# Kernel tuning notes

Measured on AMD Instinct MI355X. Metric: run time of the kernel, lower is better.

The kernel has to match this reference:

```python
import jax, jax.numpy as jnp
import numpy as np

H = 8        # attention heads
G = 8        # groupnorm groups
EPS = 1e-5

def mish(x):
    return x * jnp.tanh(jnp.logaddexp(x, 0.0))

def conv1d(x, w, b, pad):
    # x: [B,C,L], w: [O,I,K]
    y = jax.lax.conv_general_dilated(x, w, (1,), [(pad, pad)],
                                     dimension_numbers=('NCH', 'OIH', 'NCH'))
    return y + b[None, :, None]

def gn_per_step(x, gamma, beta):
    # torch code reshapes [B,C,L] -> [(B L), C] and applies GroupNorm(G, C):
    # normalize each (b, l) position over channel groups.
    B, C, L = x.shape
    xg = x.reshape(B, G, C // G, L)
    mean = xg.mean(axis=2, keepdims=True)
    var = xg.var(axis=2, keepdims=True)
    xg = (xg - mean) * jax.lax.rsqrt(var + EPS)
    return xg.reshape(B, C, L) * gamma[None, :, None] + beta[None, :, None]

def layernorm(x, g, b):
    mean = x.mean(axis=-1, keepdims=True)
    var = x.var(axis=-1, keepdims=True)
    return (x - mean) * jax.lax.rsqrt(var + EPS) * g + b


def setup_inputs() -> dict:
    key = jax.random.key(0)
    ks = jax.random.split(key, 16)
    B, Cin, Cout, L, N, CD, TD = 64, 256, 512, 512, 77, 768, 512
    w = lambda k, shape, s=0.02: (jax.random.normal(k, shape, jnp.float32) * s)
    return {
        'x': jax.random.normal(ks[0], (B, Cin, L), jnp.float32),
        't': jax.random.normal(ks[1], (B, TD), jnp.float32),
        'cond': jax.random.normal(ks[2], (B, N, CD), jnp.float32),
        'conv0_w': w(ks[3], (Cout, Cin, 5)), 'conv0_b': jnp.zeros((Cout,), jnp.float32),
        'gn0_g': jnp.ones((Cout,), jnp.float32), 'gn0_b': jnp.zeros((Cout,), jnp.float32),
        'tm_w': w(ks[4], (2 * Cout, TD)), 'tm_b': jnp.zeros((2 * Cout,), jnp.float32),
        'conv1_w': w(ks[5], (Cout, Cout, 5)), 'conv1_b': jnp.zeros((Cout,), jnp.float32),
        'gn1_g': jnp.ones((Cout,), jnp.float32), 'gn1_b': jnp.zeros((Cout,), jnp.float32),
        'res_w': w(ks[6], (Cout, Cin, 1)), 'res_b': jnp.zeros((Cout,), jnp.float32),
        'ln_x_g': jnp.ones((Cout,), jnp.float32), 'ln_x_b': jnp.zeros((Cout,), jnp.float32),
        'ln_c_g': jnp.ones((CD,), jnp.float32), 'ln_c_b': jnp.zeros((CD,), jnp.float32),
        'q_w': w(ks[7], (Cout, Cout)), 'q_b': jnp.zeros((Cout,), jnp.float32),
        'k_w': w(ks[8], (Cout, CD)), 'k_b': jnp.zeros((Cout,), jnp.float32),
        'v_w': w(ks[9], (Cout, CD)), 'v_b': jnp.zeros((Cout,), jnp.float32),
        'cond_indices': jnp.arange(B, dtype=jnp.int64 if jax.config.jax_enable_x64 else jnp.int32),
    }


def _forward(x, t, cond,
             conv0_w, conv0_b, gn0_g, gn0_b, tm_w, tm_b,
             conv1_w, conv1_b, gn1_g, gn1_b, res_w, res_b,
             ln_x_g, ln_x_b, ln_c_g, ln_c_b,
             q_w, q_b, k_w, k_b, v_w, v_b, cond_indices):
    Cout = conv0_w.shape[0]
    # ---- ResidualTemporalBlock (adagn=True) ----
    ss = jnp.einsum('bi,oi->bo', mish(t), tm_w) + tm_b        # [B, 2*Cout]
    scale = ss[:, :Cout, None]                                 # chunk dim=1
    shift = ss[:, Cout:, None]
    h = conv1d(x, conv0_w, conv0_b, pad=2)                     # [B,Cout,L]
    h = gn_per_step(h, gn0_g, gn0_b)
    h = mish(h * (1.0 + scale) + shift)                        # ada_shift_scale + Mish
    h = conv1d(h, conv1_w, conv1_b, pad=2)
    h = mish(gn_per_step(h, gn1_g, gn1_b))
    out = h + conv1d(x, res_w, res_b, pad=0)                   # residual 1x1 conv
    # ---- ResidualCrossAttentionLayer (LinearCrossAttention) ----
    xs = out[cond_indices]                                     # [Bc,Cout,L]
    xi = xs.transpose(0, 2, 1)                                 # [Bc,L,Cout]
    cs = cond[cond_indices]                                    # [Bc,N,CD]
    Bc, T, D = xi.shape
    Nn = cs.shape[1]
    Dh = D // H
    q = jnp.einsum('btl,dl->btd', layernorm(xi, ln_x_g, ln_x_b), q_w) + q_b
    cn = layernorm(cs, ln_c_g, ln_c_b)
    k = jnp.einsum('bnl,dl->bnd', cn, k_w) + k_b
    v = jnp.einsum('bnl,dl->bnd', cn, v_w) + v_b
    q = jax.nn.softmax(q.reshape(Bc, T, H, Dh), axis=-1)       # softmax over head dim
    k = jax.nn.softmax(k.reshape(Bc, Nn, H, Dh), axis=1)       # softmax over tokens
    v = v.reshape(Bc, Nn, H, Dh)
    attn = jnp.einsum('bnhd,bnhl->bhdl', k, v)                 # [Bc,H,Dh,Dh] kernel
    y = jnp.einsum('bthd,bhdl->bthl', q, attn).reshape(Bc, T, D)
    return out.at[cond_indices].add(y.transpose(0, 2, 1))


def reference(x, t, cond,
              conv0_w, conv0_b, gn0_g, gn0_b, tm_w, tm_b,
              conv1_w, conv1_b, gn1_g, gn1_b, res_w, res_b,
              ln_x_g, ln_x_b, ln_c_g, ln_c_b,
              q_w, q_b, k_w, k_b, v_w, v_b, cond_indices):
    return _forward(x, t, cond, conv0_w, conv0_b, gn0_g, gn0_b, tm_w, tm_b,
                    conv1_w, conv1_b, gn1_g, gn1_b, res_w, res_b,
                    ln_x_g, ln_x_b, ln_c_g, ln_c_b,
                    q_w, q_b, k_w, k_b, v_w, v_b, cond_indices)
```

## Files before the change

### kernel.cpp

```cpp
#include <hip/hip_runtime.h>
#include <math.h>

#define EPS 1e-5f

typedef __attribute__((ext_vector_type(8))) short short8;
typedef __attribute__((ext_vector_type(4))) float floatx4;

typedef __attribute__((address_space(1))) const void* gas1_t;
typedef __attribute__((address_space(3))) void* las3_t;

__device__ __forceinline__ void glls16(const void* g, void* l) {
    __builtin_amdgcn_global_load_lds((gas1_t)g, (las3_t)l, 16, 0, 0);
}

__device__ __forceinline__ float mishf(float x) {
    float sp = fmaxf(x, 0.0f) + log1pf(expf(-fabsf(x)));
    return x * tanhf(sp);
}
__device__ __forceinline__ unsigned short f2bf(float f) {
    unsigned int u = __float_as_uint(f);
    unsigned int r = (u + 0x7fffu + ((u >> 16) & 1u)) >> 16;
    return (unsigned short)r;
}
__device__ __forceinline__ float bf2f(unsigned short s) {
    return __uint_as_float(((unsigned int)s) << 16);
}
__device__ __forceinline__ unsigned int pk2(unsigned short a, unsigned short b) {
    return (unsigned int)a | ((unsigned int)b << 16);
}

__global__ __launch_bounds__(256) void setup_k(
        const float* __restrict__ conv0_w, const float* __restrict__ conv1_w,
        const float* __restrict__ res_w, const float* __restrict__ q_w,
        const float* __restrict__ k_w, const float* __restrict__ v_w,
        const float* __restrict__ t,
        unsigned short* __restrict__ wp0, unsigned short* __restrict__ wp1,
        unsigned short* __restrict__ wr, unsigned short* __restrict__ wq,
        unsigned short* __restrict__ wk, unsigned short* __restrict__ wvv,
        float* __restrict__ mt,
        unsigned short* __restrict__ xTp, unsigned short* __restrict__ h0Tp) {
    const int blk = blockIdx.x, tid = threadIdx.x;
    if (blk < 2560) {
        int o = blk * 256 + tid;
        int ci = o & 255, co = (o >> 8) & 511, kk = o >> 17;
        wp0[o] = f2bf(conv0_w[((size_t)co * 256 + ci) * 5 + kk]);
    } else if (blk < 7680) {
        int o = (blk - 2560) * 256 + tid;
        int ci = o & 511, co = (o >> 9) & 511, kk = o >> 18;
        wp1[o] = f2bf(conv1_w[((size_t)co * 512 + ci) * 5 + kk]);
    } else if (blk < 7808) {
        int i = (blk - 7680) * 256 + tid;
        float4 f = *(const float4*)&res_w[(size_t)i * 4];
        *(uint2*)&wr[(size_t)i * 4] =
            make_uint2(pk2(f2bf(f.x), f2bf(f.y)), pk2(f2bf(f.z), f2bf(f.w)));
    } else if (blk < 8064) {
        int i = (blk - 7808) * 256 + tid;
        float4 f = *(const float4*)&q_w[(size_t)i * 4];
        *(uint2*)&wq[(size_t)i * 4] =
            make_uint2(pk2(f2bf(f.x), f2bf(f.y)), pk2(f2bf(f.z), f2bf(f.w)));
    } else if (blk < 8448) {
        int i = (blk - 8064) * 256 + tid;
        float4 f = *(const float4*)&k_w[(size_t)i * 4];
        *(uint2*)&wk[(size_t)i * 4] =
            make_uint2(pk2(f2bf(f.x), f2bf(f.y)), pk2(f2bf(f.z), f2bf(f.w)));
    } else if (blk < 8832) {
        int i = (blk - 8448) * 256 + tid;
        float4 f = *(const float4*)&v_w[(size_t)i * 4];
        *(uint2*)&wvv[(size_t)i * 4] =
            make_uint2(pk2(f2bf(f.x), f2bf(f.y)), pk2(f2bf(f.z), f2bf(f.w)));
    } else if (blk < 8960) {
        int i = (blk - 8832) * 256 + tid;
        mt[i] = mishf(t[i]);
    } else if (blk < 8992) {
        int idx = (blk - 8960) * 256 + tid;
        int u = idx * 8;
        int c = u & 255, r4 = (u >> 8) & 3, b = u >> 10;
        int row = (r4 < 2) ? r4 : (512 + r4);
        *(uint4*)&xTp[((size_t)b * 516 + row) * 256 + c] = make_uint4(0, 0, 0, 0);
    } else {
        int idx = (blk - 8992) * 256 + tid;
        int u = idx * 8;
        int c = u & 511, r4 = (u >> 9) & 3, b = u >> 11;
        int row = (r4 < 2) ? r4 : (512 + r4);
        *(uint4*)&h0Tp[((size_t)b * 516 + row) * 512 + c] = make_uint4(0, 0, 0, 0);
    }
}

__global__ __launch_bounds__(256) void xpose_cvt(const float* __restrict__ x,
        unsigned short* __restrict__ xT) {
    __shared__ float tile[64][68];
    const int tid = threadIdx.x;
    const int l0 = blockIdx.x * 64, c0 = blockIdx.y * 64, b = blockIdx.z;
    for (int idx = tid; idx < 64 * 16; idx += 256) {
        int cr = idx >> 4, lc = (idx & 15) * 4;
        float4 f = *(const float4*)&x[((size_t)b * 256 + c0 + cr) * 512 + l0 + lc];
        tile[cr][lc] = f.x; tile[cr][lc + 1] = f.y;
        tile[cr][lc + 2] = f.z; tile[cr][lc + 3] = f.w;
    }
    __syncthreads();
    for (int idx = tid; idx < 64 * 16; idx += 256) {
        int lr = idx >> 4, cc = (idx & 15) * 4;
        *(uint2*)&xT[((size_t)b * 516 + 2 + l0 + lr) * 256 + c0 + cc] =
            make_uint2(pk2(f2bf(tile[cc][lr]), f2bf(tile[cc + 1][lr])),
                       pk2(f2bf(tile[cc + 2][lr]), f2bf(tile[cc + 3][lr])));
    }
}

template<int KD>
__global__ __launch_bounds__(256) void gemm_nt(const float* __restrict__ A,
        const float* __restrict__ W, const float* __restrict__ bias,
        float* __restrict__ C, int M, int N) {
    constexpr int ST = 20;
    __shared__ __align__(16) float As[64 * ST];
    __shared__ __align__(16) float Ws[64 * ST];
    const int tid = threadIdx.x;
    const int r0 = blockIdx.x * 64, c0 = blockIdx.y * 64;
    const int tx = tid & 15, ty = tid >> 4;
    const int lrow = tid >> 2, lk = (tid & 3) * 4;
    float acc[4][4];
#pragma unroll
    for (int i = 0; i < 4; ++i)
#pragma unroll
        for (int j = 0; j < 4; ++j) acc[i][j] = 0.f;
    for (int k0 = 0; k0 < KD; k0 += 16) {
        __syncthreads();
        *(float4*)&As[lrow * ST + lk] =
            *(const float4*)&A[(size_t)(r0 + lrow) * KD + k0 + lk];
        *(float4*)&Ws[lrow * ST + lk] =
            *(const float4*)&W[(size_t)(c0 + lrow) * KD + k0 + lk];
        __syncthreads();
#pragma unroll
        for (int kk = 0; kk < 16; kk += 4) {
            float4 av[4], wv[4];
#pragma unroll
            for (int i = 0; i < 4; ++i)
                av[i] = *(const float4*)&As[(ty + 16 * i) * ST + kk];
#pragma unroll
            for (int j = 0; j < 4; ++j)
                wv[j] = *(const float4*)&Ws[(tx + 16 * j) * ST + kk];
#pragma unroll
            for (int i = 0; i < 4; ++i)
#pragma unroll
                for (int j = 0; j < 4; ++j) {
                    acc[i][j] = fmaf(av[i].x, wv[j].x, acc[i][j]);
                    acc[i][j] = fmaf(av[i].y, wv[j].y, acc[i][j]);
                    acc[i][j] = fmaf(av[i].z, wv[j].z, acc[i][j]);
                    acc[i][j] = fmaf(av[i].w, wv[j].w, acc[i][j]);
                }
        }
    }
#pragma unroll
    for (int j = 0; j < 4; ++j) {
        int c = c0 + tx + 16 * j;
        float bv = bias[c];
#pragma unroll
        for (int i = 0; i < 4; ++i)
            C[(size_t)(r0 + ty + 16 * i) * N + c] = acc[i][j] + bv;
    }
}

template<int CI, bool FILM, bool OPAD>
__global__ __launch_bounds__(256) void conv5_mfma(
        const unsigned short* __restrict__ xb,
        const unsigned short* __restrict__ wp,
        const float* __restrict__ bias,
        const float* __restrict__ gam, const float* __restrict__ bet,
        const float* __restrict__ ss,
        unsigned short* __restrict__ outT) {
    constexpr int NC = CI / 32;
    __shared__ __align__(16) unsigned short xs[2][260 * 32];
    __shared__ __align__(16) unsigned short wsm[2][5 * 64 * 32];
    __shared__ float sgam[64], sbet[64], sbias[64], sscale[64], sshift[64];

    const int tid = threadIdx.x;
    const int l0 = blockIdx.x * 256;
    const int co0 = blockIdx.y * 64;
    const int b = blockIdx.z;
    const int lane = tid & 63;
    const int wv = tid >> 6;
    const int lq = lane & 15, qd = lane >> 4;
    const int wn = wv * 64;

    if (tid < 64) {
        int co = co0 + tid;
        sbias[tid] = bias[co];
        sgam[tid] = gam[co];
        sbet[tid] = bet[co];
        if (FILM) {
            sscale[tid] = ss[(size_t)b * 1024 + co];
            sshift[tid] = ss[(size_t)b * 1024 + 512 + co];
        }
    }

    const unsigned short* gxb = xb + ((size_t)b * 516 + l0) * CI;
    const unsigned short* gwb = wp + (size_t)co0 * CI;

    const unsigned short* xsp[5];
    const unsigned short* wsp[5];
    unsigned sdo[5];
#pragma unroll
    for (int it = 0; it < 5; ++it) {
        int task = it * 256 + tid;
        {
            int ri = task >> 2, pos = task & 3;
            int seg = pos ^ ((ri >> 1) & 3);
            xsp[it] = gxb + (size_t)ri * CI + seg * 8;
        }
        {
            int kk = task >> 8, r = task & 255;
            int col = r >> 2, pos = r & 3;
            int seg = pos ^ ((col >> 1) & 3);
            wsp[it] = gwb + ((size_t)kk * 512 + col) * CI + seg * 8;
        }
        sdo[it] = (unsigned)(it * 256 + wn) * 8;
    }
    const bool xv4 = tid < 16;

    auto stage = [&](int buf) {
#pragma unroll
        for (int it = 0; it < 5; ++it) {
            if (it < 4 || xv4) glls16(xsp[it], &xs[buf][sdo[it]]);
            xsp[it] += 32;
        }
#pragma unroll
        for (int it = 0; it < 5; ++it) {
            glls16(wsp[it], &wsm[buf][sdo[it]]);
            wsp[it] += 32;
        }
    };

    unsigned bvo[5][4], avo[5][4];
#pragma unroll
    for (int kk = 0; kk < 5; ++kk) {
#pragma unroll
        for (int j = 0; j < 4; ++j) {
            int row = wn + j * 16 + lq + kk;
            int pos = qd ^ ((row >> 1) & 3);
            bvo[kk][j] = (unsigned)(row * 32 + pos * 8) * 2u;
        }
#pragma unroll
        for (int i = 0; i < 4; ++i) {
            int crow = i * 16 + lq;
            int pos = qd ^ ((crow >> 1) & 3);
            avo[kk][i] = (unsigned)(kk * 2048 + crow * 32 + pos * 8) * 2u;
        }
    }

    floatx4 acc[4][4];
#pragma unroll
    for (int i = 0; i < 4; ++i)
#pragma unroll
        for (int j = 0; j < 4; ++j) acc[i][j] = (floatx4){0.f, 0.f, 0.f, 0.f};

    auto compute = [&](int buf) {
        const char* xr = (const char*)xs[buf];
        const char* wr_ = (const char*)wsm[buf];
#pragma unroll
        for (int kk = 0; kk < 5; ++kk) {
            short8 bvf[4];
#pragma unroll
            for (int j = 0; j < 4; ++j)
                bvf[j] = *(const short8*)(xr + bvo[kk][j]);
#pragma unroll
            for (int i = 0; i < 4; ++i) {
                short8 av = *(const short8*)(wr_ + avo[kk][i]);
#pragma unroll
                for (int j = 0; j < 4; ++j)
                    acc[i][j] = __builtin_amdgcn_mfma_f32_16x16x32_bf16(
                        av, bvf[j], acc[i][j], 0, 0, 0);
            }
        }
    };

    stage(0);
    __syncthreads();
#pragma unroll 1
    for (int c = 0; c < NC; c += 2) {
        stage(1);
        compute(0);
        __syncthreads();
        if (c + 2 < NC) stage(0);
        compute(1);
        __syncthreads();
    }

    float m_[4], rs_[4];
#pragma unroll
    for (int j = 0; j < 4; ++j) {
        float s1 = 0.f, s2 = 0.f;
#pragma unroll
        for (int i = 0; i < 4; ++i) {
            float4 bv4 = *(const float4*)&sbias[i * 16 + qd * 4];
            float ba[4] = {bv4.x, bv4.y, bv4.z, bv4.w};
#pragma unroll
            for (int r = 0; r < 4; ++r) {
                float v = acc[i][j][r] + ba[r];
                acc[i][j][r] = v;
                s1 += v; s2 += v * v;
            }
        }
        s1 += __shfl_xor(s1, 16, 64); s2 += __shfl_xor(s2, 16, 64);
        s1 += __shfl_xor(s1, 32, 64); s2 += __shfl_xor(s2, 32, 64);
        float mean = s1 * (1.f / 64.f);
        float var = s2 * (1.f / 64.f) - mean * mean;
        m_[j] = mean; rs_[j] = rsqrtf(var + EPS);
    }
#pragma unroll
    for (int j = 0; j < 4; ++j) {
        int l = l0 + wn + j * 16 + lq;
        size_t rowbase = OPAD ? (((size_t)b * 516 + 2 + l) * 512 + co0)
                              : (((size_t)b * 512 + l) * 512 + co0);
#pragma unroll
        for (int i = 0; i < 4; ++i) {
            float4 g4 = *(const float4*)&sgam[i * 16 + qd * 4];
            float4 b4 = *(const float4*)&sbet[i * 16 + qd * 4];
            float ga[4] = {g4.x, g4.y, g4.z, g4.w};
            float be[4] = {b4.x, b4.y, b4.z, b4.w};
            float sa[4] = {0, 0, 0, 0}, sh[4] = {0, 0, 0, 0};
            if (FILM) {
                float4 s4 = *(const float4*)&sscale[i * 16 + qd * 4];
                float4 h4 = *(const float4*)&sshift[i * 16 + qd * 4];
                sa[0] = s4.x; sa[1] = s4.y; sa[2] = s4.z; sa[3] = s4.w;
                sh[0] = h4.x; sh[1] = h4.y; sh[2] = h4.z; sh[3] = h4.w;
            }
            unsigned short o[4];
#pragma unroll
            for (int r = 0; r < 4; ++r) {
                float v = (acc[i][j][r] - m_[j]) * rs_[j] * ga[r] + be[r];
                if (FILM) v = v * (1.f + sa[r]) + sh[r];
                o[r] = f2bf(mishf(v));
            }
            *(uint2*)&outT[rowbase + i * 16 + qd * 4] =
                make_uint2(pk2(o[0], o[1]), pk2(o[2], o[3]));
        }
    }
}

template<int KD, int EPI, bool PADA>
__global__ __launch_bounds__(256) void gemm1_mfma(
        const unsigned short* __restrict__ A,
        const unsigned short* __restrict__ W,
        const float* __restrict__ bias,
        const unsigned short* __restrict__ addT,
        float* __restrict__ outF,
        unsigned short* __restrict__ outB,
        int Mreal) {
    constexpr int NC = KD / 32;
    __shared__ __align__(16) unsigned short xs[2][256 * 32];
    __shared__ __align__(16) unsigned short wsm[2][64 * 32];
    __shared__ float sbias[64];
    const int tid = threadIdx.x;
    const int m0 = blockIdx.x * 256;
    const int n0 = blockIdx.y * 64;
    const int lane = tid & 63;
    const int wv = tid >> 6;
    const int lq = lane & 15, qd = lane >> 4;
    const int wn = wv * 64;
    if (tid < 64) sbias[tid] = bias[n0 + tid];

    const size_t arow0 = PADA ? ((size_t)(m0 >> 9) * 516 + 2 + (m0 & 511))
                              : (size_t)m0;
    const unsigned short* gA = A + arow0 * KD;
    const unsigned short* gW = W + (size_t)n0 * KD;

    const unsigned short* xp[4];
#pragma unroll
    for (int it = 0; it < 4; ++it) {
        int task = it * 256 + tid;
        int ri = task >> 2, pos = task & 3;
        int seg = pos ^ ((ri >> 1) & 3);
        xp[it] = gA + (size_t)ri * KD + seg * 8;
    }
    const unsigned short* wpq;
    {
        int col = tid >> 2, pos = tid & 3;
        int seg = pos ^ ((col >> 1) & 3);
        wpq = gW + (size_t)col * KD + seg * 8;
    }

    auto stage = [&](int buf) {
#pragma unroll
        for (int it = 0; it < 4; ++it) {
            glls16(xp[it], &xs[buf][(unsigned)(it * 256 + wn) * 8]);
            xp[it] += 32;
        }
        glls16(wpq, &wsm[buf][(unsigned)wn * 8]);
        wpq += 32;
    };

    unsigned bvo[4], avo[4];
#pragma unroll
    for (int j = 0; j < 4; ++j) {
        int row = wn + j * 16 + lq;
        int pos = qd ^ ((row >> 1) & 3);
        bvo[j] = (unsigned)(row * 32 + pos * 8) * 2u;
    }
#pragma unroll
    for (int i = 0; i < 4; ++i) {
        int crow = i * 16 + lq;
        int pos = qd ^ ((crow >> 1) & 3);
        avo[i] = (unsigned)(crow * 32 + pos * 8) * 2u;
    }

    floatx4 acc[4][4];
#pragma unroll
    for (int i = 0; i < 4; ++i)
#pragma unroll
        for (int j = 0; j < 4; ++j) acc[i][j] = (floatx4){0.f, 0.f, 0.f, 0.f};

    auto compute = [&](int buf) {
        const char* xr = (const char*)xs[buf];
        const char* wr_ = (const char*)wsm[buf];
        short8 bvf[4];
#pragma unroll
        for (int j = 0; j < 4; ++j)
            bvf[j] = *(const short8*)(xr + bvo[j]);
#pragma unroll
        for (int i = 0; i < 4; ++i) {
            short8 av = *(const short8*)(wr_ + avo[i]);
#pragma unroll
            for (int j = 0; j < 4; ++j)
                acc[i][j] = __builtin_amdgcn_mfma_f32_16x16x32_bf16(
                    av, bvf[j], acc[i][j], 0, 0, 0);
        }
    };

    stage(0);
    __syncthreads();
#pragma unroll 1
    for (int c = 0; c < NC; c += 2) {
        stage(1);
        compute(0);
        __syncthreads();
        if (c + 2 < NC) stage(0);
        compute(1);
        __syncthreads();
    }

#pragma unroll
    for (int i = 0; i < 4; ++i) {
        float4 bv4 = *(const float4*)&sbias[i * 16 + qd * 4];
        float ba[4] = {bv4.x, bv4.y, bv4.z, bv4.w};
#pragma unroll
        for (int j = 0; j < 4; ++j)
#pragma unroll
            for (int r = 0; r < 4; ++r) acc[i][j][r] += ba[r];
    }
    if (EPI == 0) {
#pragma unroll
        for (int j = 0; j < 4; ++j) {
            int m = m0 + wn + j * 16 + lq;
#pragma unroll
            for (int i = 0; i < 4; ++i) {
                int n = n0 + i * 16 + qd * 4;
                uint2 hv = *(const uint2*)&addT[(size_t)m * 512 + n];
                float vr[4];
                vr[0] = acc[i][j][0] + bf2f((unsigned short)(hv.x & 0xffff));
                vr[1] = acc[i][j][1] + bf2f((unsigned short)(hv.x >> 16));
                vr[2] = acc[i][j][2] + bf2f((unsigned short)(hv.y & 0xffff));
                vr[3] = acc[i][j][3] + bf2f((unsigned short)(hv.y >> 16));
                *(uint2*)&outB[(size_t)m * 512 + n] =
                    make_uint2(pk2(f2bf(vr[0]), f2bf(vr[1])),
                               pk2(f2bf(vr[2]), f2bf(vr[3])));
            }
        }
    } else if (EPI == 1) {
#pragma unroll
        for (int j = 0; j < 4; ++j) {
            float mx = -3.4e38f;
#pragma unroll
            for (int i = 0; i < 4; ++i)
#pragma unroll
                for (int r = 0; r < 4; ++r) mx = fmaxf(mx, acc[i][j][r]);
            mx = fmaxf(mx, __shfl_xor(mx, 16, 64));
            mx = fmaxf(mx, __shfl_xor(mx, 32, 64));
            float s = 0.f;
#pragma unroll
            for (int i = 0; i < 4; ++i)
#pragma unroll
                for (int r = 0; r < 4; ++r) {
                    float e = expf(acc[i][j][r] - mx);
                    acc[i][j][r] = e; s += e;
                }
            s += __shfl_xor(s, 16, 64);
            s += __shfl_xor(s, 32, 64);
            float inv = 1.f / s;
            int m = m0 + wn + j * 16 + lq;
#pragma unroll
            for (int i = 0; i < 4; ++i) {
                *(uint2*)&outB[(size_t)m * 512 + n0 + i * 16 + qd * 4] =
                    make_uint2(pk2(f2bf(acc[i][j][0] * inv), f2bf(acc[i][j][1] * inv)),
                               pk2(f2bf(acc[i][j][2] * inv), f2bf(acc[i][j][3] * inv)));
            }
        }
    } else {
#pragma unroll
        for (int j = 0; j < 4; ++j) {
            int m = m0 + wn + j * 16 + lq;
            if (m < Mreal) {
#pragma unroll
                for (int i = 0; i < 4; ++i) {
                    float4 o = {acc[i][j][0], acc[i][j][1], acc[i][j][2], acc[i][j][3]};
                    *(float4*)&outF[(size_t)m * 512 + n0 + i * 16 + qd * 4] = o;
                }
            }
        }
    }
}

__global__ __launch_bounds__(256) void lnrow(const unsigned short* __restrict__ src,
        const float* __restrict__ g, const float* __restrict__ be,
        const int* __restrict__ cidx, unsigned short* __restrict__ dst) {
    const int tid = threadIdx.x;
    const int lane = tid & 63, wv = tid >> 6;
    const int row0 = blockIdx.x * 32 + wv * 8;
    for (int rr = 0; rr < 8; ++rr) {
        int m = row0 + rr;
        int b = m >> 9, t = m & 511;
        int ib = cidx[b];
        const unsigned short* sp = &src[((size_t)ib * 512 + t) * 512 + lane * 8];
        short8 u = *(const short8*)sp;
        float v[8];
        float s1 = 0.f, s2 = 0.f;
#pragma unroll
        for (int k = 0; k < 8; ++k) {
            v[k] = bf2f(((const unsigned short*)&u)[k]);
            s1 += v[k]; s2 += v[k] * v[k];
        }
#pragma unroll
        for (int o = 32; o > 0; o >>= 1) {
            s1 += __shfl_xor(s1, o, 64);
            s2 += __shfl_xor(s2, o, 64);
        }
        float mean = s1 * (1.f / 512.f);
        float var = s2 * (1.f / 512.f) - mean * mean;
        float rs = rsqrtf(var + EPS);
        float4 g0 = *(const float4*)&g[lane * 8];
        float4 g1 = *(const float4*)&g[lane * 8 + 4];
        float4 b0 = *(const float4*)&be[lane * 8];
        float4 b1 = *(const float4*)&be[lane * 8 + 4];
        float ga[8] = {g0.x, g0.y, g0.z, g0.w, g1.x, g1.y, g1.z, g1.w};
        float ba[8] = {b0.x, b0.y, b0.z, b0.w, b1.x, b1.y, b1.z, b1.w};
        unsigned short o8[8];
#pragma unroll
        for (int k = 0; k < 8; ++k)
            o8[k] = f2bf((v[k] - mean) * rs * ga[k] + ba[k]);
        *(uint4*)&dst[(size_t)m * 512 + lane * 8] =
            make_uint4(pk2(o8[0], o8[1]), pk2(o8[2], o8[3]),
                       pk2(o8[4], o8[5]), pk2(o8[6], o8[7]));
    }
}

__global__ __launch_bounds__(256) void lnc_k(const float* __restrict__ cond,
        const float* __restrict__ g, const float* __restrict__ be,
        const int* __restrict__ cidx, unsigned short* __restrict__ cn) {
    const int tid = threadIdx.x;
    const int bn = blockIdx.x;
    const int b = bn / 77, n = bn - b * 77;
    const int ib = cidx[b];
    const float* src = cond + ((size_t)ib * 77 + n) * 768;
    float v[3];
    float s = 0.f, s2 = 0.f;
#pragma unroll
    for (int i = 0; i < 3; ++i) {
        v[i] = src[tid + i * 256];
        s += v[i]; s2 += v[i] * v[i];
    }
#pragma unroll
    for (int o = 32; o > 0; o >>= 1) {
        s += __shfl_xor(s, o, 64);
        s2 += __shfl_xor(s2, o, 64);
    }
    __shared__ float r1[4], r2[4], mv[2];
    if ((tid & 63) == 0) { r1[tid >> 6] = s; r2[tid >> 6] = s2; }
    __syncthreads();
    if (tid == 0) {
        float ts = r1[0] + r1[1] + r1[2] + r1[3];
        float ts2 = r2[0] + r2[1] + r2[2] + r2[3];
        float m = ts * (1.f / 768.f);
        float var = ts2 * (1.f / 768.f) - m * m;
        mv[0] = m; mv[1] = rsqrtf(var + EPS);
    }
    __syncthreads();
    float m = mv[0], rs = mv[1];
    unsigned short* dst = cn + ((size_t)b * 77 + n) * 768;
#pragma unroll
    for (int i = 0; i < 3; ++i) {
        int c = tid + i * 256;
        dst[c] = f2bf((v[i] - m) * rs * g[c] + be[c]);
    }
}

__global__ __launch_bounds__(256) void attn_k(const float* __restrict__ k,
        const float* __restrict__ v, unsigned short* __restrict__ attnT) {
    constexpr int NS = 68;
    __shared__ __align__(16) float ks[77 * NS];
    __shared__ __align__(16) float vs[77 * NS];
    __shared__ float red[2][256];
    const int tid = threadIdx.x;
    const int b = blockIdx.x >> 3, h = blockIdx.x & 7;
    for (int idx = tid; idx < 77 * 16; idx += 256) {
        int n = idx >> 4, dq2 = (idx & 15) * 4;
        *(float4*)&ks[n * NS + dq2] =
            *(const float4*)&k[((size_t)b * 77 + n) * 512 + h * 64 + dq2];
        *(float4*)&vs[n * NS + dq2] =
            *(const float4*)&v[((size_t)b * 77 + n) * 512 + h * 64 + dq2];
    }
    __syncthreads();
    {
        const int d = tid & 63, grp = tid >> 6;
        float mx = -3.4e38f;
        for (int n = grp; n < 77; n += 4) mx = fmaxf(mx, ks[n * NS + d]);
        red[0][grp * 64 + d] = mx;
        __syncthreads();
        mx = fmaxf(fmaxf(red[0][d], red[0][64 + d]),
                   fmaxf(red[0][128 + d], red[0][192 + d]));
        float s = 0.f;
        for (int n = grp; n < 77; n += 4) {
            float e = expf(ks[n * NS + d] - mx);
            ks[n * NS + d] = e; s += e;
        }
        red[1][grp * 64 + d] = s;
        __syncthreads();
        float inv = 1.f / (red[1][d] + red[1][64 + d] + red[1][128 + d] + red[1][192 + d]);
        for (int n = grp; n < 77; n += 4) ks[n * NS + d] *= inv;
    }
    __syncthreads();
    const int e = tid & 63, dq = tid >> 6;
    float acc[16];
#pragma unroll
    for (int u = 0; u < 16; ++u) acc[u] = 0.f;
    for (int n = 0; n < 77; ++n) {
        float vv = vs[n * NS + e];
#pragma unroll
        for (int u4 = 0; u4 < 4; ++u4) {
            float4 kk = *(const float4*)&ks[n * NS + dq * 16 + u4 * 4];
            acc[u4 * 4 + 0] = fmaf(kk.x, vv, acc[u4 * 4 + 0]);
            acc[u4 * 4 + 1] = fmaf(kk.y, vv, acc[u4 * 4 + 1]);
            acc[u4 * 4 + 2] = fmaf(kk.z, vv, acc[u4 * 4 + 2]);
            acc[u4 * 4 + 3] = fmaf(kk.w, vv, acc[u4 * 4 + 3]);
        }
    }
    unsigned short ob[16];
#pragma unroll
    for (int u = 0; u < 16; ++u) ob[u] = f2bf(acc[u]);
    size_t base = (((size_t)b * 8 + h) * 64 + e) * 64 + dq * 16;
    *(uint4*)&attnT[base] = make_uint4(pk2(ob[0], ob[1]), pk2(ob[2], ob[3]),
                                       pk2(ob[4], ob[5]), pk2(ob[6], ob[7]));
    *(uint4*)&attnT[base + 8] = make_uint4(pk2(ob[8], ob[9]), pk2(ob[10], ob[11]),
                                           pk2(ob[12], ob[13]), pk2(ob[14], ob[15]));
}

__global__ __launch_bounds__(256) void yattn_final(
        const unsigned short* __restrict__ q,
        const unsigned short* __restrict__ at,
        const unsigned short* __restrict__ resT,
        const int* __restrict__ cidx, float* __restrict__ out) {
    const int tid = threadIdx.x;
    const int lane = tid & 63, wv = tid >> 6;
    const int lq = lane & 15, qd = lane >> 4;
    const int t0 = blockIdx.x * 256 + wv * 64;
    const int h = blockIdx.y, b = blockIdx.z;
    const int ib = cidx[b];
    floatx4 acc[4][4];
#pragma unroll
    for (int i = 0; i < 4; ++i)
#pragma unroll
        for (int j = 0; j < 4; ++j) acc[i][j] = (floatx4){0.f, 0.f, 0.f, 0.f};
#pragma unroll
    for (int ks = 0; ks < 2; ++ks) {
        short8 av[4], bv[4];
#pragma unroll
        for (int i = 0; i < 4; ++i)
            av[i] = *(const short8*)
                &q[((size_t)(b * 512 + t0 + i * 16 + lq)) * 512 + h * 64 + ks * 32 + qd * 8];
#pragma unroll
        for (int j = 0; j < 4; ++j)
            bv[j] = *(const short8*)
                &at[(((size_t)(b * 8 + h)) * 64 + j * 16 + lq) * 64 + ks * 32 + qd * 8];
#pragma unroll
        for (int i = 0; i < 4; ++i)
#pragma unroll
            for (int j = 0; j < 4; ++j)
                acc[i][j] = __builtin_amdgcn_mfma_f32_16x16x32_bf16(
                    av[i], bv[j], acc[i][j], 0, 0, 0);
    }
#pragma unroll
    for (int j = 0; j < 4; ++j) {
        int c = h * 64 + j * 16 + lq;
#pragma unroll
        for (int i = 0; i < 4; ++i) {
            int tb = t0 + i * 16 + qd * 4;
            float vr[4];
#pragma unroll
            for (int r = 0; r < 4; ++r)
                vr[r] = acc[i][j][r] +
                        bf2f(resT[((size_t)(ib * 512 + tb + r)) * 512 + c]);
            float4 o = {vr[0], vr[1], vr[2], vr[3]};
            *(float4*)&out[((size_t)ib * 512 + c) * 512 + tb] = o;
        }
    }
}

extern "C" void kernel_launch(void* const* d_in, const int* in_sizes, int n_in,
                              void* d_out, int out_size, void* d_ws, size_t ws_size,
                              hipStream_t stream) {
    (void)in_sizes; (void)n_in; (void)out_size; (void)ws_size;
    const float* x       = (const float*)d_in[0];
    const float* t       = (const float*)d_in[1];
    const float* cond    = (const float*)d_in[2];
    const float* conv0_w = (const float*)d_in[3];
    const float* conv0_b = (const float*)d_in[4];
    const float* gn0_g   = (const float*)d_in[5];
    const float* gn0_b   = (const float*)d_in[6];
    const float* tm_w    = (const float*)d_in[7];
    const float* tm_b    = (const float*)d_in[8];
    const float* conv1_w = (const float*)d_in[9];
    const float* conv1_b = (const float*)d_in[10];
    const float* gn1_g   = (const float*)d_in[11];
    const float* gn1_b   = (const float*)d_in[12];
    const float* res_w   = (const float*)d_in[13];
    const float* res_b   = (const float*)d_in[14];
    const float* ln_x_g  = (const float*)d_in[15];
    const float* ln_x_b  = (const float*)d_in[16];
    const float* ln_c_g  = (const float*)d_in[17];
    const float* ln_c_b  = (const float*)d_in[18];
    const float* q_w     = (const float*)d_in[19];
    const float* q_b     = (const float*)d_in[20];
    const float* k_w     = (const float*)d_in[21];
    const float* k_b     = (const float*)d_in[22];
    const float* v_w     = (const float*)d_in[23];
    const float* v_b     = (const float*)d_in[24];
    const int*   cidx    = (const int*)d_in[25];
    float* out = (float*)d_out;

    char* WS = (char*)d_ws;
    unsigned short* xTp   = (unsigned short*)(WS + 0);
    unsigned short* cnb   = (unsigned short*)(WS + 0);
    unsigned short* attnT = (unsigned short*)(WS + 8388608);
    unsigned short* h0Tp  = (unsigned short*)(WS + 16908288);
    unsigned short* xlnT  = (unsigned short*)(WS + 16908288);
    float*          kb    = (float*)(WS + 16908288);
    float*          vb    = (float*)(WS + 27000832);
    unsigned short* h1T   = (unsigned short*)(WS + 50724864);
    unsigned short* qbf   = (unsigned short*)(WS + 50724864);
    unsigned short* outTb = (unsigned short*)(WS + 84279296);
    unsigned short* wp0   = (unsigned short*)(WS + 117833728);
    unsigned short* wp1   = (unsigned short*)(WS + 119144448);
    unsigned short* wr    = (unsigned short*)(WS + 121765888);
    unsigned short* wq    = (unsigned short*)(WS + 122028032);
    unsigned short* wk    = (unsigned short*)(WS + 122552320);
    unsigned short* wvv   = (unsigned short*)(WS + 123338752);
    float*          ssb   = (float*)(WS + 124125184);
    float*          mt    = (float*)(WS + 124387328);

    setup_k<<<dim3(9056), dim3(256), 0, stream>>>(
        conv0_w, conv1_w, res_w, q_w, k_w, v_w, t,
        wp0, wp1, wr, wq, wk, wvv, mt, xTp, h0Tp);
    xpose_cvt<<<dim3(8, 4, 64), dim3(256), 0, stream>>>(x, xTp);
    gemm_nt<512><<<dim3(1, 16), dim3(256), 0, stream>>>(mt, tm_w, tm_b, ssb, 64, 1024);
    conv5_mfma<256, true, true><<<dim3(2, 8, 64), dim3(256), 0, stream>>>(
        xTp, wp0, conv0_b, gn0_g, gn0_b, ssb, h0Tp);
    conv5_mfma<512, false, false><<<dim3(2, 8, 64), dim3(256), 0, stream>>>(
        h0Tp, wp1, conv1_b, gn1_g, gn1_b, (const float*)nullptr, h1T);
    gemm1_mfma<256, 0, true><<<dim3(128, 8), dim3(256), 0, stream>>>(
        xTp, wr, res_b, h1T, (float*)nullptr, outTb, 32768);
    lnrow<<<dim3(1024), dim3(256), 0, stream>>>(outTb, ln_x_g, ln_x_b, cidx, xlnT);
    gemm1_mfma<512, 1, false><<<dim3(128, 8), dim3(256), 0, stream>>>(
        xlnT, wq, q_b, (const unsigned short*)nullptr, (float*)nullptr, qbf, 32768);
    lnc_k<<<dim3(4928), dim3(256), 0, stream>>>(cond, ln_c_g, ln_c_b, cidx, cnb);
    gemm1_mfma<768, 2, false><<<dim3(20, 8), dim3(256), 0, stream>>>(
        cnb, wk, k_b, (const unsigned short*)nullptr, kb, (unsigned short*)nullptr, 4928);
    gemm1_mfma<768, 2, false><<<dim3(20, 8), dim3(256), 0, stream>>>(
        cnb, wvv, v_b, (const unsigned short*)nullptr, vb, (unsigned short*)nullptr, 4928);
    attn_k<<<dim3(512), dim3(256), 0, stream>>>(kb, vb, attnT);
    yattn_final<<<dim3(2, 8, 64), dim3(256), 0, stream>>>(qbf, attnT, outTb, cidx, out);
}
```

Baseline: 604.7 us.

## Pre-pack weights into MFMA fragment layout and load them straight to registers

The setup kernel now writes conv and linear weights in a chunk-major layout of 32-channel slices, so each lane can fetch its MFMA A-fragment with one 16-byte global load. The conv and GEMM kernels no longer stage weights through LDS; they load them directly into registers, with the next tap prefetched while the current one computes. This halves LDS use, and launch bounds now request 3 and 4 blocks per CU to raise occupancy. In exchange, weight reads go through the cache instead of shared memory, and register pressure rises under the tighter launch bounds.

```diff
diff --git a/kernel.cpp b/kernel.cpp
--- a/kernel.cpp
+++ b/kernel.cpp
@@ -41,32 +41,44 @@
         unsigned short* __restrict__ xTp, unsigned short* __restrict__ h0Tp) {
     const int blk = blockIdx.x, tid = threadIdx.x;
     if (blk < 2560) {
-        int o = blk * 256 + tid;
-        int ci = o & 255, co = (o >> 8) & 511, kk = o >> 17;
-        wp0[o] = f2bf(conv0_w[((size_t)co * 256 + ci) * 5 + kk]);
+        int i = blk * 256 + tid;
+        int kk = i % 5, rest = i / 5;
+        int ci = rest & 255, co = rest >> 8;
+        int o = (((ci >> 5) * 5 + kk) << 14) + (co << 5) + (ci & 31);
+        wp0[o] = f2bf(conv0_w[i]);
     } else if (blk < 7680) {
-        int o = (blk - 2560) * 256 + tid;
-        int ci = o & 511, co = (o >> 9) & 511, kk = o >> 18;
-        wp1[o] = f2bf(conv1_w[((size_t)co * 512 + ci) * 5 + kk]);
+        int i = (blk - 2560) * 256 + tid;
+        int kk = i % 5, rest = i / 5;
+        int ci = rest & 511, co = rest >> 9;
+        int o = (((ci >> 5) * 5 + kk) << 14) + (co << 5) + (ci & 31);
+        wp1[o] = f2bf(conv1_w[i]);
     } else if (blk < 7808) {
         int i = (blk - 7680) * 256 + tid;
+        int n = i >> 6, ci = (i & 63) * 4;
         float4 f = *(const float4*)&res_w[(size_t)i * 4];
-        *(uint2*)&wr[(size_t)i * 4] =
+        int o = ((ci >> 5) << 14) + (n << 5) + (ci & 31);
+        *(uint2*)&wr[o] =
             make_uint2(pk2(f2bf(f.x), f2bf(f.y)), pk2(f2bf(f.z), f2bf(f.w)));
     } else if (blk < 8064) {
         int i = (blk - 7808) * 256 + tid;
+        int n = i >> 7, ci = (i & 127) * 4;
         float4 f = *(const float4*)&q_w[(size_t)i * 4];
-        *(uint2*)&wq[(size_t)i * 4] =
+        int o = ((ci >> 5) << 14) + (n << 5) + (ci & 31);
+        *(uint2*)&wq[o] =
             make_uint2(pk2(f2bf(f.x), f2bf(f.y)), pk2(f2bf(f.z), f2bf(f.w)));
     } else if (blk < 8448) {
         int i = (blk - 8064) * 256 + tid;
+        int n = i / 192, r = i - n * 192, ci = r * 4;
         float4 f = *(const float4*)&k_w[(size_t)i * 4];
-        *(uint2*)&wk[(size_t)i * 4] =
+        int o = ((ci >> 5) << 14) + (n << 5) + (ci & 31);
+        *(uint2*)&wk[o] =
             make_uint2(pk2(f2bf(f.x), f2bf(f.y)), pk2(f2bf(f.z), f2bf(f.w)));
     } else if (blk < 8832) {
         int i = (blk - 8448) * 256 + tid;
+        int n = i / 192, r = i - n * 192, ci = r * 4;
         float4 f = *(const float4*)&v_w[(size_t)i * 4];
-        *(uint2*)&wvv[(size_t)i * 4] =
+        int o = ((ci >> 5) << 14) + (n << 5) + (ci & 31);
+        *(uint2*)&wvv[o] =
             make_uint2(pk2(f2bf(f.x), f2bf(f.y)), pk2(f2bf(f.z), f2bf(f.w)));
     } else if (blk < 8960) {
         int i = (blk - 8832) * 256 + tid;
@@ -160,7 +172,7 @@
 }
 
 template<int CI, bool FILM, bool OPAD>
-__global__ __launch_bounds__(256) void conv5_mfma(
+__global__ __launch_bounds__(256, 3) void conv5_mfma(
         const unsigned short* __restrict__ xb,
         const unsigned short* __restrict__ wp,
         const float* __restrict__ bias,
@@ -169,7 +181,6 @@
         unsigned short* __restrict__ outT) {
     constexpr int NC = CI / 32;
     __shared__ __align__(16) unsigned short xs[2][260 * 32];
-    __shared__ __align__(16) unsigned short wsm[2][5 * 64 * 32];
     __shared__ float sgam[64], sbet[64], sbias[64], sscale[64], sshift[64];
 
     const int tid = threadIdx.x;
@@ -193,58 +204,26 @@
     }
 
     const unsigned short* gxb = xb + ((size_t)b * 516 + l0) * CI;
-    const unsigned short* gwb = wp + (size_t)co0 * CI;
 
     const unsigned short* xsp[5];
-    const unsigned short* wsp[5];
-    unsigned sdo[5];
 #pragma unroll
     for (int it = 0; it < 5; ++it) {
         int task = it * 256 + tid;
-        {
-            int ri = task >> 2, pos = task & 3;
-            int seg = pos ^ ((ri >> 1) & 3);
-            xsp[it] = gxb + (size_t)ri * CI + seg * 8;
-        }
-        {
-            int kk = task >> 8, r = task & 255;
-            int col = r >> 2, pos = r & 3;
-            int seg = pos ^ ((col >> 1) & 3);
-            wsp[it] = gwb + ((size_t)kk * 512 + col) * CI + seg * 8;
-        }
-        sdo[it] = (unsigned)(it * 256 + wn) * 8;
+        int ri = task >> 2, pos = task & 3;
+        int seg = pos ^ ((ri >> 1) & 3);
+        xsp[it] = gxb + (size_t)ri * CI + seg * 8;
     }
     const bool xv4 = tid < 16;
 
     auto stage = [&](int buf) {
 #pragma unroll
         for (int it = 0; it < 5; ++it) {
-            if (it < 4 || xv4) glls16(xsp[it], &xs[buf][sdo[it]]);
+            if (it < 4 || xv4) glls16(xsp[it], &xs[buf][(unsigned)(it * 256 + wn) * 8]);
             xsp[it] += 32;
         }
-#pragma unroll
-        for (int it = 0; it < 5; ++it) {
-            glls16(wsp[it], &wsm[buf][sdo[it]]);
-            wsp[it] += 32;
-        }
     };
 
-    unsigned bvo[5][4], avo[5][4];
-#pragma unroll
-    for (int kk = 0; kk < 5; ++kk) {
-#pragma unroll
-        for (int j = 0; j < 4; ++j) {
-            int row = wn + j * 16 + lq + kk;
-            int pos = qd ^ ((row >> 1) & 3);
-            bvo[kk][j] = (unsigned)(row * 32 + pos * 8) * 2u;
-        }
-#pragma unroll
-        for (int i = 0; i < 4; ++i) {
-            int crow = i * 16 + lq;
-            int pos = qd ^ ((crow >> 1) & 3);
-            avo[kk][i] = (unsigned)(kk * 2048 + crow * 32 + pos * 8) * 2u;
-        }
-    }
+    const unsigned short* pA = wp + (size_t)(co0 + lq) * 32 + qd * 8;
 
     floatx4 acc[4][4];
 #pragma unroll
@@ -252,36 +231,52 @@
 #pragma unroll
         for (int j = 0; j < 4; ++j) acc[i][j] = (floatx4){0.f, 0.f, 0.f, 0.f};
 
-    auto compute = [&](int buf) {
+    auto chunk = [&](int c, int buf, bool more) {
+        const unsigned short* pAc = pA + (size_t)c * (5 * 16384);
+        short8 a0[4], a1[4];
+#pragma unroll
+        for (int i = 0; i < 4; ++i)
+            a0[i] = *(const short8*)(pAc + i * 512);
+        if (more) stage(buf ^ 1);
+#pragma unroll
+        for (int i = 0; i < 4; ++i)
+            a1[i] = *(const short8*)(pAc + 16384 + i * 512);
         const char* xr = (const char*)xs[buf];
-        const char* wr_ = (const char*)wsm[buf];
 #pragma unroll
         for (int kk = 0; kk < 5; ++kk) {
             short8 bvf[4];
 #pragma unroll
-            for (int j = 0; j < 4; ++j)
-                bvf[j] = *(const short8*)(xr + bvo[kk][j]);
-#pragma unroll
-            for (int i = 0; i < 4; ++i) {
-                short8 av = *(const short8*)(wr_ + avo[kk][i]);
+            for (int j = 0; j < 4; ++j) {
+                int row = wn + j * 16 + lq + kk;
+                int pos = qd ^ ((row >> 1) & 3);
+                bvf[j] = *(const short8*)(xr + (unsigned)(row * 32 + pos * 8) * 2u);
+            }
+            short8 acur[4];
+#pragma unroll
+            for (int i = 0; i < 4; ++i) acur[i] = (kk & 1) ? a1[i] : a0[i];
+            if (kk < 3) {
+#pragma unroll
+                for (int i = 0; i < 4; ++i) {
+                    short8 tmp = *(const short8*)(pAc + (kk + 2) * 16384 + i * 512);
+                    if (kk & 1) a1[i] = tmp; else a0[i] = tmp;
+                }
+            }
+#pragma unroll
+            for (int i = 0; i < 4; ++i)
 #pragma unroll
                 for (int j = 0; j < 4; ++j)
                     acc[i][j] = __builtin_amdgcn_mfma_f32_16x16x32_bf16(
-                        av, bvf[j], acc[i][j], 0, 0, 0);
-            }
-        }
+                        acur[i], bvf[j], acc[i][j], 0, 0, 0);
+        }
+        __syncthreads();
     };
 
     stage(0);
     __syncthreads();
 #pragma unroll 1
     for (int c = 0; c < NC; c += 2) {
-        stage(1);
-        compute(0);
-        __syncthreads();
-        if (c + 2 < NC) stage(0);
-        compute(1);
-        __syncthreads();
+        chunk(c, 0, true);
+        chunk(c + 1, 1, c + 2 < NC);
     }
 
     float m_[4], rs_[4];
@@ -337,7 +332,7 @@
 }
 
 template<int KD, int EPI, bool PADA>
-__global__ __launch_bounds__(256) void gemm1_mfma(
+__global__ __launch_bounds__(256, 4) void gemm1_mfma(
         const unsigned short* __restrict__ A,
         const unsigned short* __restrict__ W,
         const float* __restrict__ bias,
@@ -347,7 +342,6 @@
         int Mreal) {
     constexpr int NC = KD / 32;
     __shared__ __align__(16) unsigned short xs[2][256 * 32];
-    __shared__ __align__(16) unsigned short wsm[2][64 * 32];
     __shared__ float sbias[64];
     const int tid = threadIdx.x;
     const int m0 = blockIdx.x * 256;
@@ -361,7 +355,6 @@
     const size_t arow0 = PADA ? ((size_t)(m0 >> 9) * 516 + 2 + (m0 & 511))
                               : (size_t)m0;
     const unsigned short* gA = A + arow0 * KD;
-    const unsigned short* gW = W + (size_t)n0 * KD;
 
     const unsigned short* xp[4];
 #pragma unroll
@@ -371,12 +364,6 @@
         int seg = pos ^ ((ri >> 1) & 3);
         xp[it] = gA + (size_t)ri * KD + seg * 8;
     }
-    const unsigned short* wpq;
-    {
-        int col = tid >> 2, pos = tid & 3;
-        int seg = pos ^ ((col >> 1) & 3);
-        wpq = gW + (size_t)col * KD + seg * 8;
-    }
 
     auto stage = [&](int buf) {
 #pragma unroll
@@ -384,23 +371,17 @@
             glls16(xp[it], &xs[buf][(unsigned)(it * 256 + wn) * 8]);
             xp[it] += 32;
         }
-        glls16(wpq, &wsm[buf][(unsigned)wn * 8]);
-        wpq += 32;
     };
 
-    unsigned bvo[4], avo[4];
+    const unsigned short* pA = W + (size_t)(n0 + lq) * 32 + qd * 8;
+
+    unsigned bvo[4];
 #pragma unroll
     for (int j = 0; j < 4; ++j) {
         int row = wn + j * 16 + lq;
         int pos = qd ^ ((row >> 1) & 3);
         bvo[j] = (unsigned)(row * 32 + pos * 8) * 2u;
     }
-#pragma unroll
-    for (int i = 0; i < 4; ++i) {
-        int crow = i * 16 + lq;
-        int pos = qd ^ ((crow >> 1) & 3);
-        avo[i] = (unsigned)(crow * 32 + pos * 8) * 2u;
-    }
 
     floatx4 acc[4][4];
 #pragma unroll
@@ -408,33 +389,33 @@
 #pragma unroll
         for (int j = 0; j < 4; ++j) acc[i][j] = (floatx4){0.f, 0.f, 0.f, 0.f};
 
-    auto compute = [&](int buf) {
+    auto chunk = [&](int c, int buf, bool more) {
+        short8 av[4];
+        const unsigned short* pAc = pA + (size_t)c * 16384;
+#pragma unroll
+        for (int i = 0; i < 4; ++i)
+            av[i] = *(const short8*)(pAc + i * 512);
+        if (more) stage(buf ^ 1);
         const char* xr = (const char*)xs[buf];
-        const char* wr_ = (const char*)wsm[buf];
         short8 bvf[4];
 #pragma unroll
         for (int j = 0; j < 4; ++j)
             bvf[j] = *(const short8*)(xr + bvo[j]);
 #pragma unroll
-        for (int i = 0; i < 4; ++i) {
-            short8 av = *(const short8*)(wr_ + avo[i]);
+        for (int i = 0; i < 4; ++i)
 #pragma unroll
             for (int j = 0; j < 4; ++j)
                 acc[i][j] = __builtin_amdgcn_mfma_f32_16x16x32_bf16(
-                    av, bvf[j], acc[i][j], 0, 0, 0);
-        }
+                    av[i], bvf[j], acc[i][j], 0, 0, 0);
+        __syncthreads();
     };
 
     stage(0);
     __syncthreads();
 #pragma unroll 1
     for (int c = 0; c < NC; c += 2) {
-        stage(1);
-        compute(0);
-        __syncthreads();
-        if (c + 2 < NC) stage(0);
-        compute(1);
-        __syncthreads();
+        chunk(c, 0, true);
+        chunk(c + 1, 1, c + 2 < NC);
     }
 
 #pragma unroll
```

Result: slower. 657.3 us (+8.7%).

## Deepen global-to-LDS prefetch pipeline with partial vmcnt waits in conv/GEMM loops

Applied to the files above, without the earlier changes.

Both MFMA main loops now stage two chunks ahead before the loop and, on each iteration, issue the next global_load_lds for the freed buffer. They then wait only on the older loads using explicit s_waitcnt vmcnt counts instead of a full __syncthreads drain. Compute is also wrapped in s_setprio to favour MFMA issue. This is meant to keep loads in flight across the barrier so memory latency overlaps compute. The hard-coded vmcnt values depend on the exact number of loads per stage, so if that count changes the kernel can race or stall.

```diff
diff --git a/kernel.cpp b/kernel.cpp
--- a/kernel.cpp
+++ b/kernel.cpp
@@ -273,15 +273,23 @@
     };
 
     stage(0);
+    stage(1);
     __syncthreads();
 #pragma unroll 1
-    for (int c = 0; c < NC; c += 2) {
-        stage(1);
-        compute(0);
-        __syncthreads();
-        if (c + 2 < NC) stage(0);
-        compute(1);
-        __syncthreads();
+    for (int c = 0; c < NC; ++c) {
+        __builtin_amdgcn_s_setprio(1);
+        compute(c & 1);
+        __builtin_amdgcn_s_setprio(0);
+        if (c + 1 < NC) {
+            __builtin_amdgcn_s_barrier();
+            if (c + 2 < NC) {
+                stage(c & 1);
+                asm volatile("s_waitcnt vmcnt(9)" ::: "memory");
+            } else {
+                asm volatile("s_waitcnt vmcnt(0)" ::: "memory");
+            }
+            __builtin_amdgcn_s_barrier();
+        }
     }
 
     float m_[4], rs_[4];
@@ -426,15 +434,23 @@
     };
 
     stage(0);
+    stage(1);
     __syncthreads();
 #pragma unroll 1
-    for (int c = 0; c < NC; c += 2) {
-        stage(1);
-        compute(0);
-        __syncthreads();
-        if (c + 2 < NC) stage(0);
-        compute(1);
-        __syncthreads();
+    for (int c = 0; c < NC; ++c) {
+        __builtin_amdgcn_s_setprio(1);
+        compute(c & 1);
+        __builtin_amdgcn_s_setprio(0);
+        if (c + 1 < NC) {
+            __builtin_amdgcn_s_barrier();
+            if (c + 2 < NC) {
+                stage(c & 1);
+                asm volatile("s_waitcnt vmcnt(5)" ::: "memory");
+            } else {
+                asm volatile("s_waitcnt vmcnt(0)" ::: "memory");
+            }
+            __builtin_amdgcn_s_barrier();
+        }
     }
 
 #pragma unroll
```

Measured after the change: 620.9 us. 2.7% more time.
